# Kernel tuning notes

Hardware: AMD Instinct MI355X
Metric: run time of the kernel (lower is better)

## Reference

```python
import jax, jax.numpy as jnp
import numpy as np

DIM = 512

def setup_inputs() -> dict:
    key = jax.random.key(0)
    k1, k2 = jax.random.split(key)
    pq = jax.random.normal(k1, (65536, 2 * DIM), dtype=jnp.float32)
    A = jax.random.normal(k2, (DIM, DIM), dtype=jnp.float32)
    return {"pq": pq, "A": A}

def reference(pq, A):
    # up_or_low == 'up': p' = p + (A + A^T) q ; q' = q
    S = A + A.T  # symmetric (dim, dim)
    p = pq[..., :DIM]
    q = pq[..., DIM:]
    # (A+A^T) q for each row: since S is symmetric, q @ S == q @ S^T
    pterm = jnp.einsum('bd,ed->be', q, S)  # matches mv(S, q) per row
    return jnp.concatenate([p + pterm, q], axis=-1)
```

## Files before the change

kernel.cpp:

```cpp
#include <hip/hip_runtime.h>
#include <hip/hip_bf16.h>

#define DIM 512
#define BM 32

typedef __bf16 bf16x8 __attribute__((ext_vector_type(8)));
typedef float f32x16 __attribute__((ext_vector_type(16)));
typedef float f32x4  __attribute__((ext_vector_type(4)));

union B128 { uint4 u; bf16x8 v; };
union PK  { ushort4 h[2]; uint4 u; };
union F4  { float4 hip; f32x4 cv; };

__device__ __forceinline__ unsigned short f2bf(float f) {
    union { __hip_bfloat16 b; unsigned short u; } c;
    c.b = __float2bfloat16(f);
    return c.u;
}

__device__ __forceinline__ void nt_store4(const float4& v, float* p) {
    F4 u; u.hip = v;
    __builtin_nontemporal_store(u.cv, (f32x4*)p);
}

__global__ void prep_s_kernel(const float* __restrict__ A,
                              unsigned short* __restrict__ Sf) {
    const int c   = blockIdx.x * 256 + threadIdx.x;
    const int l   = c & 63;
    const int ks  = (c >> 6) & 31;
    const int nt2 = c >> 11;
    const int e   = nt2 * 32 + (l & 31);
    const int d0  = ks * 16 + (l >> 5) * 8;
    float4 r0 = *(const float4*)(A + (size_t)e * DIM + d0);
    float4 r1 = *(const float4*)(A + (size_t)e * DIM + d0 + 4);
    float cl[8];
    #pragma unroll
    for (int j = 0; j < 8; ++j) cl[j] = A[(size_t)(d0 + j) * DIM + e];
    ushort4 o0, o1;
    o0.x = f2bf(r0.x + cl[0]); o0.y = f2bf(r0.y + cl[1]);
    o0.z = f2bf(r0.z + cl[2]); o0.w = f2bf(r0.w + cl[3]);
    o1.x = f2bf(r1.x + cl[4]); o1.y = f2bf(r1.y + cl[5]);
    o1.z = f2bf(r1.z + cl[6]); o1.w = f2bf(r1.w + cl[7]);
    *(ushort4*)(Sf + (size_t)c * 8)     = o0;
    *(ushort4*)(Sf + (size_t)c * 8 + 4) = o1;
}

__global__ __launch_bounds__(256, 4) void fused_gemm_kernel(
        const float* __restrict__ pq,
        const unsigned short* __restrict__ Sf,
        float* __restrict__ out) {
    __shared__ __align__(16) unsigned char smem[32768];
    unsigned short* As = (unsigned short*)smem;
    float*          Cs = (float*)smem;

    const int t = threadIdx.x;
    const int l = t & 63;
    const int w = t >> 6;
    const int lane31 = l & 31;
    const int half   = l >> 5;
    const int m0 = blockIdx.x * BM;

    float4 qv[16];
    #pragma unroll
    for (int p = 0; p < 8; ++p) {
        const int c    = p * 256 + t;
        const int row  = c >> 6;
        const int col0 = (c & 63) * 8;
        const size_t goff = (size_t)(m0 + row) * (2 * DIM) + DIM + col0;
        qv[2 * p]     = *(const float4*)(pq + goff);
        qv[2 * p + 1] = *(const float4*)(pq + goff + 4);
    }
    #pragma unroll
    for (int p = 0; p < 8; ++p) {
        const int c    = p * 256 + t;
        const int row  = c >> 6;
        const int w6   = c & 63;
        const int ks   = w6 >> 1;
        const int hi   = w6 & 1;
        const int col0 = w6 * 8;
        const size_t goff = (size_t)(m0 + row) * (2 * DIM) + DIM + col0;
        nt_store4(qv[2 * p],     out + goff);
        nt_store4(qv[2 * p + 1], out + goff + 4);
        PK pk;
        pk.h[0].x = f2bf(qv[2 * p].x);     pk.h[0].y = f2bf(qv[2 * p].y);
        pk.h[0].z = f2bf(qv[2 * p].z);     pk.h[0].w = f2bf(qv[2 * p].w);
        pk.h[1].x = f2bf(qv[2 * p + 1].x); pk.h[1].y = f2bf(qv[2 * p + 1].y);
        pk.h[1].z = f2bf(qv[2 * p + 1].z); pk.h[1].w = f2bf(qv[2 * p + 1].w);
        const int f = (row + 32 * hi) ^ (ks & 7);
        *(uint4*)(As + (size_t)(ks * 64 + f) * 8) = pk.u;
    }
    __syncthreads();

    f32x16 acc[4];
    #pragma unroll
    for (int nt = 0; nt < 4; ++nt)
        #pragma unroll
        for (int r = 0; r < 16; ++r) acc[nt][r] = 0.0f;

    #pragma unroll 2
    for (int ks = 0; ks < 32; ++ks) {
        B128 a;
        a.u = *(const uint4*)(As + (size_t)(ks * 64 + (l ^ (ks & 7))) * 8);
        #pragma unroll
        for (int nt = 0; nt < 4; ++nt) {
            const int nt2 = nt * 4 + w;
            B128 b;
            b.u = *(const uint4*)(Sf + (size_t)((nt2 * 32 + ks) * 64 + l) * 8);
            acc[nt] = __builtin_amdgcn_mfma_f32_32x32x16_bf16(a.v, b.v, acc[nt], 0, 0, 0);
        }
    }

    #pragma unroll
    for (int h = 0; h < 2; ++h) {
        float4 pv[8];
        #pragma unroll
        for (int it = 0; it < 8; ++it) {
            const int u   = it * 256 + t;
            const int row = u >> 6;
            const int c0  = (u & 63) * 4;
            const size_t goff = (size_t)(m0 + row) * (2 * DIM) + 256 * h + c0;
            pv[it] = *(const float4*)(pq + goff);
        }
        __syncthreads();
        #pragma unroll
        for (int i = 0; i < 2; ++i) {
            const int nt = 2 * h + i;
            const int colb = 128 * i + 32 * w + lane31;
            #pragma unroll
            for (int r = 0; r < 16; ++r) {
                const int row = 4 * half + (r & 3) + 8 * (r >> 2);
                Cs[row * 256 + colb] = acc[nt][r];
            }
        }
        __syncthreads();
        #pragma unroll
        for (int it = 0; it < 8; ++it) {
            const int u   = it * 256 + t;
            const int row = u >> 6;
            const int c0  = (u & 63) * 4;
            float4 v = *(const float4*)(Cs + row * 256 + c0);
            const size_t goff = (size_t)(m0 + row) * (2 * DIM) + 256 * h + c0;
            v.x += pv[it].x; v.y += pv[it].y; v.z += pv[it].z; v.w += pv[it].w;
            nt_store4(v, out + goff);
        }
    }
}

extern "C" void kernel_launch(void* const* d_in, const int* in_sizes, int n_in,
                              void* d_out, int out_size, void* d_ws, size_t ws_size,
                              hipStream_t stream) {
    const float* pq = (const float*)d_in[0];
    const float* A  = (const float*)d_in[1];
    float* out = (float*)d_out;
    unsigned short* Sf = (unsigned short*)d_ws;

    prep_s_kernel<<<(DIM * DIM / 8) / 256, 256, 0, stream>>>(A, Sf);
    fused_gemm_kernel<<<65536 / BM, 256, 0, stream>>>(pq, Sf, out);
}
```

Before: 580.8 us.

## Split q staging into two rounds, raise occupancy bound, drop nontemporal stores

Splits the q load/convert/store prologue into two rounds of four tiles, separated by a scheduling barrier, so fewer registers stay live at once. Raises the launch-bounds occupancy hint from 4 to 5 blocks per CU. Replaces the nontemporal stores with ordinary float4 stores. Each round now has fewer loads in flight, which may expose more memory latency, and the higher occupancy target could force register spills.

```diff
diff --git a/kernel.cpp b/kernel.cpp
--- a/kernel.cpp
+++ b/kernel.cpp
@@ -6,21 +6,14 @@
 
 typedef __bf16 bf16x8 __attribute__((ext_vector_type(8)));
 typedef float f32x16 __attribute__((ext_vector_type(16)));
-typedef float f32x4  __attribute__((ext_vector_type(4)));
 
 union B128 { uint4 u; bf16x8 v; };
 union PK  { ushort4 h[2]; uint4 u; };
-union F4  { float4 hip; f32x4 cv; };
 
 __device__ __forceinline__ unsigned short f2bf(float f) {
     union { __hip_bfloat16 b; unsigned short u; } c;
     c.b = __float2bfloat16(f);
     return c.u;
-}
-
-__device__ __forceinline__ void nt_store4(const float4& v, float* p) {
-    F4 u; u.hip = v;
-    __builtin_nontemporal_store(u.cv, (f32x4*)p);
 }
 
 __global__ void prep_s_kernel(const float* __restrict__ A,
@@ -45,7 +38,7 @@
     *(ushort4*)(Sf + (size_t)c * 8 + 4) = o1;
 }
 
-__global__ __launch_bounds__(256, 4) void fused_gemm_kernel(
+__global__ __launch_bounds__(256, 5) void fused_gemm_kernel(
         const float* __restrict__ pq,
         const unsigned short* __restrict__ Sf,
         float* __restrict__ out) {
@@ -60,34 +53,40 @@
     const int half   = l >> 5;
     const int m0 = blockIdx.x * BM;
 
-    float4 qv[16];
     #pragma unroll
-    for (int p = 0; p < 8; ++p) {
-        const int c    = p * 256 + t;
-        const int row  = c >> 6;
-        const int col0 = (c & 63) * 8;
-        const size_t goff = (size_t)(m0 + row) * (2 * DIM) + DIM + col0;
-        qv[2 * p]     = *(const float4*)(pq + goff);
-        qv[2 * p + 1] = *(const float4*)(pq + goff + 4);
-    }
-    #pragma unroll
-    for (int p = 0; p < 8; ++p) {
-        const int c    = p * 256 + t;
-        const int row  = c >> 6;
-        const int w6   = c & 63;
-        const int ks   = w6 >> 1;
-        const int hi   = w6 & 1;
-        const int col0 = w6 * 8;
-        const size_t goff = (size_t)(m0 + row) * (2 * DIM) + DIM + col0;
-        nt_store4(qv[2 * p],     out + goff);
-        nt_store4(qv[2 * p + 1], out + goff + 4);
-        PK pk;
-        pk.h[0].x = f2bf(qv[2 * p].x);     pk.h[0].y = f2bf(qv[2 * p].y);
-        pk.h[0].z = f2bf(qv[2 * p].z);     pk.h[0].w = f2bf(qv[2 * p].w);
-        pk.h[1].x = f2bf(qv[2 * p + 1].x); pk.h[1].y = f2bf(qv[2 * p + 1].y);
-        pk.h[1].z = f2bf(qv[2 * p + 1].z); pk.h[1].w = f2bf(qv[2 * p + 1].w);
-        const int f = (row + 32 * hi) ^ (ks & 7);
-        *(uint4*)(As + (size_t)(ks * 64 + f) * 8) = pk.u;
+    for (int rnd = 0; rnd < 2; ++rnd) {
+        float4 qv[8];
+        #pragma unroll
+        for (int pp = 0; pp < 4; ++pp) {
+            const int p    = rnd * 4 + pp;
+            const int c    = p * 256 + t;
+            const int row  = c >> 6;
+            const int col0 = (c & 63) * 8;
+            const size_t goff = (size_t)(m0 + row) * (2 * DIM) + DIM + col0;
+            qv[2 * pp]     = *(const float4*)(pq + goff);
+            qv[2 * pp + 1] = *(const float4*)(pq + goff + 4);
+        }
+        __builtin_amdgcn_sched_barrier(0);
+        #pragma unroll
+        for (int pp = 0; pp < 4; ++pp) {
+            const int p    = rnd * 4 + pp;
+            const int c    = p * 256 + t;
+            const int row  = c >> 6;
+            const int w6   = c & 63;
+            const int ks   = w6 >> 1;
+            const int hi   = w6 & 1;
+            const int col0 = w6 * 8;
+            const size_t goff = (size_t)(m0 + row) * (2 * DIM) + DIM + col0;
+            *(float4*)(out + goff)     = qv[2 * pp];
+            *(float4*)(out + goff + 4) = qv[2 * pp + 1];
+            PK pk;
+            pk.h[0].x = f2bf(qv[2 * pp].x);     pk.h[0].y = f2bf(qv[2 * pp].y);
+            pk.h[0].z = f2bf(qv[2 * pp].z);     pk.h[0].w = f2bf(qv[2 * pp].w);
+            pk.h[1].x = f2bf(qv[2 * pp + 1].x); pk.h[1].y = f2bf(qv[2 * pp + 1].y);
+            pk.h[1].z = f2bf(qv[2 * pp + 1].z); pk.h[1].w = f2bf(qv[2 * pp + 1].w);
+            const int f = (row + 32 * hi) ^ (ks & 7);
+            *(uint4*)(As + (size_t)(ks * 64 + f) * 8) = pk.u;
+        }
     }
     __syncthreads();
 
@@ -141,7 +140,7 @@
             float4 v = *(const float4*)(Cs + row * 256 + c0);
             const size_t goff = (size_t)(m0 + row) * (2 * DIM) + 256 * h + c0;
             v.x += pv[it].x; v.y += pv[it].y; v.z += pv[it].z; v.w += pv[it].w;
-            nt_store4(v, out + goff);
+            *(float4*)(out + goff) = v;
         }
     }
 }
```

Result: faster. 554.4 us (-4.5%).
